# Kernel optimization log

Measured on AMD Instinct MI355X. Metric: run time of the kernel, lower is better.

Reference implementation:

```python
import jax, jax.numpy as jnp
import numpy as np

N = 8192
E = 262144
NEG = 0.2  # leaky_relu negative slope used throughout


def setup_inputs() -> dict:
    key = jax.random.key(0)
    def rn(i, shape, s=0.05):
        return jax.random.normal(jax.random.fold_in(key, i), shape, jnp.float32) * s
    d = {}
    d["x"] = jax.random.normal(jax.random.fold_in(key, 0), (N, 64), jnp.float32)
    d["edge_index"] = jax.random.randint(jax.random.fold_in(key, 1), (2, E), 0, N, dtype=jnp.int32)
    wshapes = {"w0": (64, 256), "as0": (4, 64), "ad0": (4, 64), "r0": (64, 256),
               "w1": (256, 256), "as1": (4, 64), "ad1": (4, 64), "r1": (256, 256),
               "w2": (256, 64), "as2": (1, 64), "ad2": (1, 64), "r2": (256, 64),
               "p0": (256, 64), "p1": (256, 64),
               "qw": (64, 64), "kw": (64, 64), "vw": (64, 64), "ow": (64, 64),
               "m1w": (64, 64), "m2w": (64, 32), "m3w": (32, 10)}
    for i, (nm, sh) in enumerate(wshapes.items()):
        d[nm] = rn(i + 2, sh)
    for nm, dim in [("g0", 256), ("g1", 256), ("g2", 64)]:
        d[nm] = jnp.ones((dim,), jnp.float32)
    for nm, dim in [("be0", 256), ("be1", 256), ("be2", 64), ("b0", 256), ("b1", 256), ("b2", 64),
                    ("qb", 64), ("kb", 64), ("vb", 64), ("ob", 64), ("m1b", 64), ("m2b", 32), ("m3b", 10)]:
        d[nm] = jnp.zeros((dim,), jnp.float32)
    return d


def _forward(edge_index, x, w0, as0, ad0, b0, g0, be0, r0,
             w1, as1, ad1, b1, g1, be1, r1,
             w2, as2, ad2, b2, g2, be2, r2,
             p0, p1, qw, qb, kw, kb, vw, vb, ow, ob,
             m1w, m1b, m2w, m2b, m3w, m3b):
    n = x.shape[0]
    loops = jnp.arange(n, dtype=edge_index.dtype)
    src = jnp.concatenate([edge_index[0], loops])  # add_self_loops=True
    dst = jnp.concatenate([edge_index[1], loops])

    def gat(h, w, a_s, a_d, b, heads):
        hw = (h @ w).reshape(n, heads, 64)  # [N, H, C]
        # PyG GATConv: e_ij = leaky_relu(att_src . h_j + att_dst . h_i), softmax over in-edges of i
        e = jax.nn.leaky_relu(jnp.sum(hw * a_s, -1)[src] + jnp.sum(hw * a_d, -1)[dst], NEG)  # [Etot, H]
        m = jax.ops.segment_max(e, dst, num_segments=n)
        ex = jnp.exp(e - m[dst])
        den = jax.ops.segment_sum(ex, dst, num_segments=n)
        alpha = ex / (den[dst] + 1e-16)
        out = jax.ops.segment_sum(hw[src] * alpha[:, :, None], dst, num_segments=n)
        return out.reshape(n, heads * 64) + b

    def bn(h, g, bta):  # BatchNorm1d, batch statistics (training-mode math)
        mu = jnp.mean(h, 0)
        var = jnp.var(h, 0)
        return (h - mu) * jax.lax.rsqrt(var + 1e-5) * g + bta

    outs = []
    h = x
    for (w, a_s, a_d, b, g, bt, r, heads) in [
            (w0, as0, ad0, b0, g0, be0, r0, 4),
            (w1, as1, ad1, b1, g1, be1, r1, 4),
            (w2, as2, ad2, b2, g2, be2, r2, 1)]:
        res = h @ r
        h = bn(gat(h, w, a_s, a_d, b, heads), g, bt) + res  # shapes always match here
        h = jax.nn.leaky_relu(h, NEG)
        outs.append(h)

    # JumpingKnowledge 'max' after projecting first two layers to hidden dim
    z = jnp.maximum(jnp.maximum(outs[0] @ p0, outs[1] @ p1), outs[2])  # [N, 64]

    # MultiHeadSelfAttention over all nodes (batch=1 implicit), 2 heads, head_dim=32
    q = (z @ qw + qb).reshape(n, 2, 32)
    k = (z @ kw + kb).reshape(n, 2, 32)
    v = (z @ vw + vb).reshape(n, 2, 32)
    attn = jax.nn.softmax(jnp.einsum('nhd,mhd->hnm', q, k) * (32 ** -0.5), axis=-1)
    z = jnp.einsum('hnm,mhd->nhd', attn, v).reshape(n, 64) @ ow + ob

    # MLP head (no data.batch -> GlobalAttention pool skipped)
    z = jax.nn.leaky_relu(z @ m1w + m1b, NEG)
    z = jax.nn.leaky_relu(z @ m2w + m2b, NEG)
    return z @ m3w + m3b


def reference(x, edge_index, w0, as0, ad0, b0, g0, be0, r0,
              w1, as1, ad1, b1, g1, be1, r1,
              w2, as2, ad2, b2, g2, be2, r2,
              p0, p1, qw, qb, kw, kb, vw, vb, ow, ob,
              m1w, m1b, m2w, m2b, m3w, m3b):
    return _forward(edge_index, x, w0, as0, ad0, b0, g0, be0, r0,
                    w1, as1, ad1, b1, g1, be1, r1,
                    w2, as2, ad2, b2, g2, be2, r2,
                    p0, p1, qw, qb, kw, kb, vw, vb, ow, ob,
                    m1w, m1b, m2w, m2b, m3w, m3b)
```

## Files before the change

kernel.cpp:

```cpp
#include <hip/hip_runtime.h>
#include <hip/hip_bf16.h>


#define NEG 0.2f
#define LOG2E 1.4426950408889634f

__device__ __forceinline__ float leaky(float v) { return v > 0.f ? v : NEG * v; }

__device__ __forceinline__ unsigned bf16u(float x) {
    unsigned u = __float_as_uint(x);
    u += 0x7FFFu + ((u >> 16) & 1u);
    return u >> 16;
}
__device__ __forceinline__ unsigned fmap(float f) {
    unsigned u = __float_as_uint(f);
    return (u & 0x80000000u) ? ~u : (u | 0x80000000u);
}
__device__ __forceinline__ float funmap(unsigned u) {
    unsigned b = (u & 0x80000000u) ? (u & 0x7FFFFFFFu) : ~u;
    return __uint_as_float(b);
}
__device__ __forceinline__ float fexp2(float x) {
#if __has_builtin(__builtin_amdgcn_exp2f)
    return __builtin_amdgcn_exp2f(x);
#else
    return exp2f(x);
#endif
}
__device__ __forceinline__ unsigned cvtpk(float lo, float hi) {
    unsigned r;
    asm("v_cvt_pk_bf16_f32 %0, %1, %2" : "=v"(r) : "v"(lo), "v"(hi));
    return r;
}

typedef __attribute__((ext_vector_type(8))) short bf16x8;
typedef __attribute__((ext_vector_type(16))) float f32x16;
typedef __attribute__((ext_vector_type(4))) unsigned uint4v;

__device__ __forceinline__ void split1(float v, unsigned& hb, unsigned& lb) {
    hb = bf16u(v);
    float hf = __uint_as_float(hb << 16);
    lb = bf16u(v - hf);
}

__global__ void split_rows(const float* __restrict__ in,
                           unsigned short* __restrict__ hi,
                           unsigned short* __restrict__ lo, int total4)
{
    int i = blockIdx.x * 256 + threadIdx.x;
    if (i >= total4) return;
    float4 v = ((const float4*)in)[i];
    float vv[4] = {v.x, v.y, v.z, v.w};
    ushort4 h, l;
#pragma unroll
    for (int j = 0; j < 4; ++j) {
        unsigned hb, lb;
        split1(vv[j], hb, lb);
        (&h.x)[j] = (unsigned short)hb;
        (&l.x)[j] = (unsigned short)lb;
    }
    ((ushort4*)hi)[i] = h;
    ((ushort4*)lo)[i] = l;
}

struct WEnt { const float* src; unsigned short* hi; unsigned short* lo; int K; int N; };
struct WArr { WEnt e[15]; };

__global__ void split_weights(WArr a)
{
    WEnt w = a.e[blockIdx.y];
    int id = blockIdx.x * 256 + threadIdx.x;
    if (id >= w.K * w.N) return;
    int k = id / w.N, n = id - k * w.N;
    unsigned hb, lb;
    split1(w.src[id], hb, lb);
    w.hi[(size_t)n * w.K + k] = (unsigned short)hb;
    w.lo[(size_t)n * w.K + k] = (unsigned short)lb;
}

__global__ __launch_bounds__(256) void gemm_mfma(
    const unsigned short* __restrict__ Ahi, const unsigned short* __restrict__ Alo,
    const unsigned short* __restrict__ Bhi, const unsigned short* __restrict__ Blo,
    const float* __restrict__ bias, float* __restrict__ C,
    unsigned short* __restrict__ Chi, unsigned short* __restrict__ Clo,
    const float* __restrict__ jkB, const float* __restrict__ jkC,
    unsigned* __restrict__ kmaxDst, const float* __restrict__ kbias,
    int M, int N, int K, int act)
{
    const int lane = threadIdx.x & 63, wid = threadIdx.x >> 6;
    const int hb4 = lane >> 5, lq = lane & 31;
    const int row0 = blockIdx.y * 64 + (wid >> 1) * 32;
    const int col0 = blockIdx.x * 64 + (wid & 1) * 32;
    const size_t abase = (size_t)(row0 + lq) * K + hb4 * 8;
    const size_t bbase = (size_t)(col0 + lq) * K + hb4 * 8;
    f32x16 acc0, acc1;
#pragma unroll
    for (int r = 0; r < 16; ++r) { acc0[r] = 0.f; acc1[r] = 0.f; }
    for (int k0 = 0; k0 < K; k0 += 16) {
        bf16x8 a_h = *(const bf16x8*)(Ahi + abase + k0);
        bf16x8 a_l = *(const bf16x8*)(Alo + abase + k0);
        bf16x8 b_h = *(const bf16x8*)(Bhi + bbase + k0);
        bf16x8 b_l = *(const bf16x8*)(Blo + bbase + k0);
        acc0 = __builtin_amdgcn_mfma_f32_32x32x16_bf16(a_h, b_h, acc0, 0, 0, 0);
        acc1 = __builtin_amdgcn_mfma_f32_32x32x16_bf16(a_l, b_h, acc1, 0, 0, 0);
        acc1 = __builtin_amdgcn_mfma_f32_32x32x16_bf16(a_h, b_l, acc1, 0, 0, 0);
    }
    int col = col0 + lq;
    if (col >= N) return;
    float bs = bias ? bias[col] : 0.f;
    float kmx = 0.f;
#pragma unroll
    for (int r = 0; r < 16; ++r) {
        int row = row0 + (r & 3) + 8 * (r >> 2) + 4 * hb4;
        float v = acc0[r] + acc1[r] + bs;
        if (act) v = leaky(v);
        if (jkB) v = fmaxf(fmaxf(v, jkB[(size_t)row * N + col]),
                           jkC[(size_t)row * N + col]);
        if (kmaxDst) kmx = fmaxf(kmx, fabsf(v + kbias[col & 63]));
        if (C) C[(size_t)row * N + col] = v;
        if (Chi) {
            unsigned hh, ll;
            split1(v, hh, ll);
            Chi[(size_t)row * N + col] = (unsigned short)hh;
            Clo[(size_t)row * N + col] = (unsigned short)ll;
        }
    }
    if (kmaxDst && col >= 64 && col < 128)
        atomicMax(&kmaxDst[col - 64], __float_as_uint(kmx));
}

template <int H>
__global__ __launch_bounds__(256) void sd_kernel(
    const float* __restrict__ hwres, int S,
    const float* __restrict__ a_s, const float* __restrict__ a_d,
    float* __restrict__ sval, float* __restrict__ dval,
    unsigned* __restrict__ svmax, int Nn)
{
    int i = blockIdx.x * 256 + threadIdx.x;
    int n = i / H, h = i & (H - 1);
    const float4* row = (const float4*)(hwres + (size_t)n * S + h * 64);
    const float4* as4 = (const float4*)(a_s + h * 64);
    const float4* ad4 = (const float4*)(a_d + h * 64);
    float s = 0.f, d = 0.f;
#pragma unroll
    for (int c = 0; c < 16; ++c) {
        float4 x = row[c], a = as4[c], b = ad4[c];
        s += x.x * a.x + x.y * a.y + x.z * a.z + x.w * a.w;
        d += x.x * b.x + x.y * b.y + x.z * b.z + x.w * b.w;
    }
    s *= LOG2E;
    d *= LOG2E;
    sval[i] = s;
    dval[i] = d;
    float m = s;
#pragma unroll
    for (int off = H; off < 64; off <<= 1) m = fmaxf(m, __shfl_xor(m, off));
    if ((threadIdx.x & 63) < H) atomicMax(&svmax[h], fmap(m));
}

__global__ void csr_count(const int* __restrict__ ei, int* __restrict__ cnt, int E) {
    int i = blockIdx.x * 256 + threadIdx.x;
    if (i < E) atomicAdd(&cnt[ei[E + i]], 1);
}

__global__ __launch_bounds__(256) void csr_scan(const int* __restrict__ cnt,
                                                int* __restrict__ rowptr,
                                                int* __restrict__ fill, int Nn)
{
    __shared__ int part[256];
    int t = threadIdx.x;
    int loc[32];
    int s = 0;
#pragma unroll
    for (int j = 0; j < 32; ++j) { loc[j] = s; s += cnt[t * 32 + j]; }
    part[t] = s;
    __syncthreads();
    for (int d = 1; d < 256; d <<= 1) {
        int v = (t >= d) ? part[t - d] : 0;
        __syncthreads();
        part[t] += v;
        __syncthreads();
    }
    int off = (t > 0) ? part[t - 1] : 0;
#pragma unroll
    for (int j = 0; j < 32; ++j) {
        int v = off + loc[j];
        rowptr[t * 32 + j] = v;
        fill[t * 32 + j] = v;
    }
    if (t == 255) rowptr[Nn] = part[255];
}

__global__ void csr_scatter(const int* __restrict__ ei, int* __restrict__ fill,
                            int* __restrict__ srcidx, int E) {
    int i = blockIdx.x * 256 + threadIdx.x;
    if (i < E) {
        int d = ei[E + i];
        int p = atomicAdd(&fill[d], 1);
        srcidx[p] = ei[i];
    }
}

__global__ __launch_bounds__(256) void gat_gather4(
    const int* __restrict__ rowptr, const int* __restrict__ srcidx,
    const float* __restrict__ hwres, int S,
    const float* __restrict__ sval, const float* __restrict__ dval,
    const unsigned* __restrict__ svmax, float* __restrict__ gout, int Nn)
{
    const int node = blockIdx.x * 4 + (threadIdx.x >> 6);
    const int lane = threadIdx.x & 63;
    const int hd = lane >> 4;
    const int cb = lane * 4;
    const int beg = rowptr[node], end = rowptr[node + 1];
    const float dv = dval[node * 4 + hd];
    const float B = leaky(funmap(svmax[hd]) + dv);
    float p = fexp2(leaky(sval[node * 4 + hd] + dv) - B);
    float l = p;
    float4 hv = *(const float4*)(hwres + (size_t)node * S + cb);
    float a0 = p * hv.x, a1 = p * hv.y, a2 = p * hv.z, a3 = p * hv.w;
    int i = beg;
    for (; i + 4 <= end; i += 4) {
        int s0 = srcidx[i], s1 = srcidx[i + 1];
        int s2 = srcidx[i + 2], s3 = srcidx[i + 3];
        float p0 = fexp2(leaky(sval[s0 * 4 + hd] + dv) - B);
        float p1 = fexp2(leaky(sval[s1 * 4 + hd] + dv) - B);
        float p2 = fexp2(leaky(sval[s2 * 4 + hd] + dv) - B);
        float p3 = fexp2(leaky(sval[s3 * 4 + hd] + dv) - B);
        float4 r0 = *(const float4*)(hwres + (size_t)s0 * S + cb);
        float4 r1 = *(const float4*)(hwres + (size_t)s1 * S + cb);
        float4 r2 = *(const float4*)(hwres + (size_t)s2 * S + cb);
        float4 r3 = *(const float4*)(hwres + (size_t)s3 * S + cb);
        l += (p0 + p1) + (p2 + p3);
        a0 += p0 * r0.x + p1 * r1.x + p2 * r2.x + p3 * r3.x;
        a1 += p0 * r0.y + p1 * r1.y + p2 * r2.y + p3 * r3.y;
        a2 += p0 * r0.z + p1 * r1.z + p2 * r2.z + p3 * r3.z;
        a3 += p0 * r0.w + p1 * r1.w + p2 * r2.w + p3 * r3.w;
    }
    for (; i < end; ++i) {
        int s0 = srcidx[i];
        float p0 = fexp2(leaky(sval[s0 * 4 + hd] + dv) - B);
        float4 r0 = *(const float4*)(hwres + (size_t)s0 * S + cb);
        l += p0;
        a0 += p0 * r0.x; a1 += p0 * r0.y; a2 += p0 * r0.z; a3 += p0 * r0.w;
    }
    float inv = 1.f / l;
    *(float4*)(gout + (size_t)node * 256 + cb) =
        make_float4(a0 * inv, a1 * inv, a2 * inv, a3 * inv);
}

__global__ __launch_bounds__(256) void gat_gather1(
    const int* __restrict__ rowptr, const int* __restrict__ srcidx,
    const float* __restrict__ hwres, int S,
    const float* __restrict__ sval, const float* __restrict__ dval,
    const unsigned* __restrict__ svmax, float* __restrict__ gout, int Nn)
{
    const int node = blockIdx.x * 4 + (threadIdx.x >> 6);
    const int lane = threadIdx.x & 63;
    const int beg = rowptr[node], end = rowptr[node + 1];
    const float dv = dval[node];
    const float B = leaky(funmap(svmax[0]) + dv);
    float p = fexp2(leaky(sval[node] + dv) - B);
    float l = p;
    float acc = p * hwres[(size_t)node * S + lane];
    int i = beg;
    for (; i + 4 <= end; i += 4) {
        int s0 = srcidx[i], s1 = srcidx[i + 1];
        int s2 = srcidx[i + 2], s3 = srcidx[i + 3];
        float p0 = fexp2(leaky(sval[s0] + dv) - B);
        float p1 = fexp2(leaky(sval[s1] + dv) - B);
        float p2 = fexp2(leaky(sval[s2] + dv) - B);
        float p3 = fexp2(leaky(sval[s3] + dv) - B);
        l += (p0 + p1) + (p2 + p3);
        acc += p0 * hwres[(size_t)s0 * S + lane] + p1 * hwres[(size_t)s1 * S + lane]
             + p2 * hwres[(size_t)s2 * S + lane] + p3 * hwres[(size_t)s3 * S + lane];
    }
    for (; i < end; ++i) {
        int s0 = srcidx[i];
        float p0 = fexp2(leaky(sval[s0] + dv) - B);
        l += p0;
        acc += p0 * hwres[(size_t)s0 * S + lane];
    }
    gout[(size_t)node * 64 + lane] = acc / l;
}

__global__ void bn_partial(const float* __restrict__ gout, double* __restrict__ sums,
                           int Nn, int C)
{
    int t = threadIdx.x;
    int c = t % C, sub = t / C, nsub = blockDim.x / C;
    int rbase = blockIdx.x * 32;
    double s = 0.0, sq = 0.0;
    for (int r = rbase + sub; r < rbase + 32; r += nsub) {
        float x = gout[(size_t)r * C + c];
        s += x;
        sq += (double)x * x;
    }
    atomicAdd(&sums[c], s);
    atomicAdd(&sums[C + c], sq);
}

__global__ void bn_res_act(const float* __restrict__ gout,
                           const float* __restrict__ hwres, int S, int logC,
                           const double* __restrict__ bnsum, double invN,
                           const float* __restrict__ g, const float* __restrict__ be,
                           float* __restrict__ outp,
                           unsigned short* __restrict__ shi,
                           unsigned short* __restrict__ slo, int total)
{
    int i = blockIdx.x * blockDim.x + threadIdx.x;
    if (i >= total) return;
    int C = 1 << logC;
    int c = i & (C - 1), row = i >> logC;
    double m = bnsum[c] * invN;
    double var = bnsum[C + c] * invN - m * m;
    float mu = (float)m;
    float rstd = (float)(1.0 / sqrt(var + 1e-5));
    float v = (gout[i] - mu) * rstd * g[c] + be[c]
              + hwres[(size_t)row * S + C + c];
    v = leaky(v);
    if (outp) outp[i] = v;
    if (shi) {
        unsigned hb, lb;
        split1(v, hb, lb);
        shi[i] = (unsigned short)hb;
        slo[i] = (unsigned short)lb;
    }
}

__global__ void qkv_prep(const float* __restrict__ zqkv,
                         const float* __restrict__ qb, const float* __restrict__ kb,
                         const float* __restrict__ vb,
                         const unsigned* __restrict__ kmaxu,
                         __hip_bfloat16* __restrict__ Qb, __hip_bfloat16* __restrict__ Kb,
                         __hip_bfloat16* __restrict__ Vf, float* __restrict__ bound,
                         int N)
{
    int idx = blockIdx.x * 256 + threadIdx.x;
    if (idx < 2 * N) {
        int h = idx / N, row = idx - h * N;
        const float scale = 0.17677669529663687f * LOG2E;
        const float* qp = zqkv + (size_t)row * 192 + h * 32;
        const float* kp = zqkv + (size_t)row * 192 + 64 + h * 32;
        float b = 0.f;
        unsigned qo[16], ko[16];
#pragma unroll
        for (int i = 0; i < 16; ++i) {
            float q0 = (qp[2 * i] + qb[h * 32 + 2 * i]) * scale;
            float q1 = (qp[2 * i + 1] + qb[h * 32 + 2 * i + 1]) * scale;
            float k0 = kp[2 * i] + kb[h * 32 + 2 * i];
            float k1 = kp[2 * i + 1] + kb[h * 32 + 2 * i + 1];
            b += fabsf(q0) * __uint_as_float(kmaxu[h * 32 + 2 * i]);
            b += fabsf(q1) * __uint_as_float(kmaxu[h * 32 + 2 * i + 1]);
            qo[i] = bf16u(q0) | (bf16u(q1) << 16);
            ko[i] = bf16u(k0) | (bf16u(k1) << 16);
        }
        uint4* qd = (uint4*)(Qb + (size_t)idx * 32);
        uint4* kd = (uint4*)(Kb + (size_t)idx * 32);
#pragma unroll
        for (int i = 0; i < 4; ++i) {
            qd[i] = make_uint4(qo[4 * i], qo[4 * i + 1], qo[4 * i + 2], qo[4 * i + 3]);
            kd[i] = make_uint4(ko[4 * i], ko[4 * i + 1], ko[4 * i + 2], ko[4 * i + 3]);
        }
        bound[idx] = b;
    } else {
        int j = idx - 2 * N;
        if (j >= 2 * (N >> 4) * 64) return;
        int lane = j & 63;
        int g = (j >> 6) % (N >> 4);
        int h = (j >> 6) / (N >> 4);
        int hi = lane >> 5;
        int kbase = g * 16 + 4 * hi;
        int d = (lane & 31) + h * 32;
        float bd = vb[d];
        unsigned o[4];
#pragma unroll
        for (int i = 0; i < 4; ++i) {
            int r0 = kbase + ((2 * i) & 3) + 8 * (i >> 1);
            unsigned u0 = bf16u(zqkv[(size_t)r0 * 192 + 128 + d] + bd);
            unsigned u1 = bf16u(zqkv[(size_t)(r0 + 1) * 192 + 128 + d] + bd);
            o[i] = u0 | (u1 << 16);
        }
        *(uint4*)(Vf + (size_t)j * 8) = make_uint4(o[0], o[1], o[2], o[3]);
    }
}

__global__ __launch_bounds__(256) void attn_mfma(
    const __hip_bfloat16* __restrict__ Qb, const __hip_bfloat16* __restrict__ Kb,
    const __hip_bfloat16* __restrict__ Vf, const float* __restrict__ bound,
    float* __restrict__ pl, __hip_bfloat16* __restrict__ pacc,
    int N, int nchunk, int chunksz)
{
    const int lane = threadIdx.x & 63;
    const int wid = threadIdx.x >> 6;
    const int hi = lane >> 5, lq = lane & 31;
    const int chunk = blockIdx.x;
    const int qtile = blockIdx.y * 4 + wid;
    const int head = qtile / (N >> 5);
    const int q0 = (qtile % (N >> 5)) * 32;
    const int kbase = chunk * chunksz;

    const size_t qrow = (size_t)head * N + q0 + lq;
    const bf16x8 qf0 = *(const bf16x8*)(Qb + qrow * 32 + hi * 8);
    const bf16x8 qf1 = *(const bf16x8*)(Qb + qrow * 32 + hi * 8 + 16);
    const float bnd = bound[qrow];

    f32x16 oacc;
#pragma unroll
    for (int r = 0; r < 16; ++r) oacc[r] = 0.f;
    float lsum = 0.f;

    for (int kt = kbase; kt < kbase + chunksz; kt += 32) {
        const size_t krow = (size_t)head * N + kt + lq;
        const bf16x8 kf0 = *(const bf16x8*)(Kb + krow * 32 + hi * 8);
        const bf16x8 kf1 = *(const bf16x8*)(Kb + krow * 32 + hi * 8 + 16);
        f32x16 s;
#pragma unroll
        for (int r = 0; r < 16; ++r) s[r] = 0.f;
        s = __builtin_amdgcn_mfma_f32_32x32x16_bf16(kf0, qf0, s, 0, 0, 0);
        s = __builtin_amdgcn_mfma_f32_32x32x16_bf16(kf1, qf1, s, 0, 0, 0);
        const __hip_bfloat16* vfb =
            Vf + (((size_t)head * (N >> 4) + (kt >> 4)) * 64 + lane) * 8;
        const bf16x8 vf0 = *(const bf16x8*)vfb;
        const bf16x8 vf1 = *(const bf16x8*)(vfb + 64 * 8);

        float p[16];
#pragma unroll
        for (int r = 0; r < 16; ++r) p[r] = fexp2(s[r] - bnd);
        float ls = 0.f;
#pragma unroll
        for (int r = 0; r < 16; ++r) ls += p[r];
        lsum += ls;

        uint4v b1, b2;
        b1[0] = cvtpk(p[0], p[1]);
        b1[1] = cvtpk(p[2], p[3]);
        b1[2] = cvtpk(p[4], p[5]);
        b1[3] = cvtpk(p[6], p[7]);
        b2[0] = cvtpk(p[8], p[9]);
        b2[1] = cvtpk(p[10], p[11]);
        b2[2] = cvtpk(p[12], p[13]);
        b2[3] = cvtpk(p[14], p[15]);
        oacc = __builtin_amdgcn_mfma_f32_32x32x16_bf16(
            vf0, __builtin_bit_cast(bf16x8, b1), oacc, 0, 0, 0);
        oacc = __builtin_amdgcn_mfma_f32_32x32x16_bf16(
            vf1, __builtin_bit_cast(bf16x8, b2), oacc, 0, 0, 0);
    }
    lsum += __shfl_xor(lsum, 32);
    const size_t hr = (size_t)head * N + q0 + lq;
    if (hi == 0) pl[hr * nchunk + chunk] = lsum;
    __hip_bfloat16* pb = pacc + (hr * nchunk + chunk) * 32;
#pragma unroll
    for (int rg = 0; rg < 4; ++rg) {
        unsigned lo = cvtpk(oacc[rg * 4 + 0], oacc[rg * 4 + 1]);
        unsigned hw2 = cvtpk(oacc[rg * 4 + 2], oacc[rg * 4 + 3]);
        *(uint2*)(pb + rg * 8 + hi * 4) = make_uint2(lo, hw2);
    }
}

__global__ void attn_combine(const float* __restrict__ pl,
                             const __hip_bfloat16* __restrict__ pacc,
                             unsigned short* __restrict__ shi,
                             unsigned short* __restrict__ slo, int N, int nchunk)
{
    int i = blockIdx.x * blockDim.x + threadIdx.x;
    if (i >= 2 * N * 32) return;
    int hr = i >> 5, cc = i & 31;
    float l = 0.f, a = 0.f;
    for (int c = 0; c < nchunk; ++c) {
        l += pl[(size_t)hr * nchunk + c];
        a += __bfloat162float(pacc[((size_t)hr * nchunk + c) * 32 + cc]);
    }
    int head = hr / N, row = hr - head * N;
    float v = a / l;
    size_t oi = (size_t)row * 64 + head * 32 + cc;
    unsigned hb, lb;
    split1(v, hb, lb);
    shi[oi] = (unsigned short)hb;
    slo[oi] = (unsigned short)lb;
}

extern "C" void kernel_launch(void* const* d_in, const int* in_sizes, int n_in,
                              void* d_out, int out_size, void* d_ws, size_t ws_size,
                              hipStream_t stream)
{
    const float* x = (const float*)d_in[0];
    const int* ei = (const int*)d_in[1];
    const float* w[3]   = {(const float*)d_in[2], (const float*)d_in[6],  (const float*)d_in[10]};
    const float* as_[3] = {(const float*)d_in[3], (const float*)d_in[7],  (const float*)d_in[11]};
    const float* ad_[3] = {(const float*)d_in[4], (const float*)d_in[8],  (const float*)d_in[12]};
    const float* rw[3]  = {(const float*)d_in[5], (const float*)d_in[9],  (const float*)d_in[13]};
    const float* p0 = (const float*)d_in[14];
    const float* p1 = (const float*)d_in[15];
    const float* qw = (const float*)d_in[16];
    const float* kw = (const float*)d_in[17];
    const float* vw = (const float*)d_in[18];
    const float* ow = (const float*)d_in[19];
    const float* m1w = (const float*)d_in[20];
    const float* m2w = (const float*)d_in[21];
    const float* m3w = (const float*)d_in[22];
    const float* g_[3]  = {(const float*)d_in[23], (const float*)d_in[24], (const float*)d_in[25]};
    const float* be_[3] = {(const float*)d_in[26], (const float*)d_in[27], (const float*)d_in[28]};
    const float* qb  = (const float*)d_in[32];
    const float* kb  = (const float*)d_in[33];
    const float* vb  = (const float*)d_in[34];
    const float* ob  = (const float*)d_in[35];
    const float* m1b = (const float*)d_in[36];
    const float* m2b = (const float*)d_in[37];
    const float* m3b = (const float*)d_in[38];

    const int N = in_sizes[0] / 64;
    const int E = in_sizes[1] / 2;

    float* ws = (float*)d_ws;
    size_t off = 0;
    auto alloc = [&](size_t n) {
        float* p = ws + off;
        off += (n + 255) & ~(size_t)255;
        return p;
    };
    float* hwres = alloc((size_t)N * 512);
    float* gout  = alloc((size_t)N * 256);
    unsigned short* sChi = (unsigned short*)alloc((size_t)N * 128);
    unsigned short* sClo = (unsigned short*)alloc((size_t)N * 128);
    float* h2   = alloc((size_t)N * 64);
    float* sval = alloc((size_t)N * 4);
    float* dval = alloc((size_t)N * 4);
    size_t ms_begin = off;
    int* cnt = (int*)alloc(N);
    double* bnsum = (double*)alloc(3 * 1024);
    unsigned* kmaxu = (unsigned*)alloc(64);
    unsigned* svmax = (unsigned*)alloc(16);
    size_t ms_end = off;
    int* rowptr = (int*)alloc(N + 256);
    int* fill   = (int*)alloc(N);
    int* srcidx = (int*)alloc(E);
    unsigned short* sAhi = (unsigned short*)alloc((size_t)N * 128);
    unsigned short* sAlo = (unsigned short*)alloc((size_t)N * 128);
    unsigned short* sBhi = (unsigned short*)alloc((size_t)N * 32);
    unsigned short* sBlo = (unsigned short*)alloc((size_t)N * 32);
    unsigned short* G0h = (unsigned short*)alloc(512 * 64 / 2);
    unsigned short* G0l = (unsigned short*)alloc(512 * 64 / 2);
    unsigned short* G1h = (unsigned short*)alloc(512 * 256 / 2);
    unsigned short* G1l = (unsigned short*)alloc(512 * 256 / 2);
    unsigned short* G2h = (unsigned short*)alloc(128 * 256 / 2);
    unsigned short* G2l = (unsigned short*)alloc(128 * 256 / 2);
    unsigned short* P0h = (unsigned short*)alloc(64 * 256 / 2);
    unsigned short* P0l = (unsigned short*)alloc(64 * 256 / 2);
    unsigned short* P1h = (unsigned short*)alloc(64 * 256 / 2);
    unsigned short* P1l = (unsigned short*)alloc(64 * 256 / 2);
    unsigned short* Gqh = (unsigned short*)alloc(192 * 64 / 2);
    unsigned short* Gql = (unsigned short*)alloc(192 * 64 / 2);
    unsigned short* Owh = (unsigned short*)alloc(64 * 64 / 2);
    unsigned short* Owl = (unsigned short*)alloc(64 * 64 / 2);
    unsigned short* M1h = (unsigned short*)alloc(64 * 64 / 2);
    unsigned short* M1l = (unsigned short*)alloc(64 * 64 / 2);
    unsigned short* M2h = (unsigned short*)alloc(64 * 64 / 2);
    unsigned short* M2l = (unsigned short*)alloc(64 * 64 / 2);
    unsigned short* M3h = (unsigned short*)alloc(64 * 32 / 2);
    unsigned short* M3l = (unsigned short*)alloc(64 * 32 / 2);
    float* zqkv = hwres;
    __hip_bfloat16* pacc = (__hip_bfloat16*)(hwres + (size_t)N * 192);
    float* tA = gout;
    float* tB = gout + (size_t)N * 64;
    const int NCHUNK = 8;
    __hip_bfloat16* Qb = (__hip_bfloat16*)sChi;
    __hip_bfloat16* Kb = Qb + (size_t)2 * N * 32;
    __hip_bfloat16* Vf = Kb + (size_t)2 * N * 32;
    float* boundArr = (float*)(Vf + (size_t)2 * N * 32);
    float* pl = h2;

    {
        WArr wa;
        wa.e[0]  = WEnt{w[0],  G0h,              G0l,              64, 256};
        wa.e[1]  = WEnt{rw[0], G0h + 256 * 64,   G0l + 256 * 64,   64, 256};
        wa.e[2]  = WEnt{w[1],  G1h,              G1l,              256, 256};
        wa.e[3]  = WEnt{rw[1], G1h + 256 * 256,  G1l + 256 * 256,  256, 256};
        wa.e[4]  = WEnt{w[2],  G2h,              G2l,              256, 64};
        wa.e[5]  = WEnt{rw[2], G2h + 64 * 256,   G2l + 64 * 256,   256, 64};
        wa.e[6]  = WEnt{p0,    P0h,              P0l,              256, 64};
        wa.e[7]  = WEnt{p1,    P1h,              P1l,              256, 64};
        wa.e[8]  = WEnt{qw,    Gqh,              Gql,              64, 64};
        wa.e[9]  = WEnt{kw,    Gqh + 64 * 64,    Gql + 64 * 64,    64, 64};
        wa.e[10] = WEnt{vw,    Gqh + 128 * 64,   Gql + 128 * 64,   64, 64};
        wa.e[11] = WEnt{ow,    Owh,              Owl,              64, 64};
        wa.e[12] = WEnt{m1w,   M1h,              M1l,              64, 64};
        wa.e[13] = WEnt{m2w,   M2h,              M2l,              64, 32};
        wa.e[14] = WEnt{m3w,   M3h,              M3l,              32, 10};
        split_weights<<<dim3(256, 15), 256, 0, stream>>>(wa);
    }
    hipMemsetAsync(ws + ms_begin, 0, (ms_end - ms_begin) * 4, stream);
    csr_count<<<(E + 255) / 256, 256, 0, stream>>>(ei, cnt, E);
    csr_scan<<<1, 256, 0, stream>>>(cnt, rowptr, fill, N);
    csr_scatter<<<(E + 255) / 256, 256, 0, stream>>>(ei, fill, srcidx, E);
    split_rows<<<(N * 64 / 4 + 255) / 256, 256, 0, stream>>>(x, sAhi, sAlo, N * 64 / 4);

    auto gemmM = [&](const unsigned short* Ah, const unsigned short* Al,
                     const unsigned short* Bh, const unsigned short* Bl,
                     const float* bias, float* C, unsigned short* Chi,
                     unsigned short* Clo, const float* jkB, const float* jkC,
                     unsigned* kmx, const float* kbias,
                     int M, int Nc, int K, int act) {
        dim3 grid((Nc + 63) / 64, M / 64);
        gemm_mfma<<<grid, 256, 0, stream>>>(Ah, Al, Bh, Bl, bias, C, Chi, Clo,
                                            jkB, jkC, kmx, kbias, M, Nc, K, act);
    };

    const unsigned short* inh[3] = {sAhi, sChi, sAhi};
    const unsigned short* inl[3] = {sAlo, sClo, sAlo};
    unsigned short* outh[3] = {sChi, sAhi, nullptr};
    unsigned short* outl[3] = {sClo, sAlo, nullptr};
    const unsigned short* Gh[3] = {G0h, G1h, G2h};
    const unsigned short* Gl[3] = {G0l, G1l, G2l};
    int Ksz[3] = {64, 256, 256}, Csz[3] = {256, 256, 64}, logC[3] = {8, 8, 6};
    int Hh[3] = {4, 4, 1};

    for (int l = 0; l < 3; ++l) {
        int C = Csz[l], S = 2 * C;
        gemmM(inh[l], inl[l], Gh[l], Gl[l], nullptr, hwres, nullptr, nullptr,
              nullptr, nullptr, nullptr, nullptr, N, S, Ksz[l], 0);
        if (Hh[l] == 4) {
            sd_kernel<4><<<N * 4 / 256, 256, 0, stream>>>(
                hwres, S, as_[l], ad_[l], sval, dval, svmax + l * 4, N);
            gat_gather4<<<N / 4, 256, 0, stream>>>(
                rowptr, srcidx, hwres, S, sval, dval, svmax + l * 4, gout, N);
        } else {
            sd_kernel<1><<<N / 256, 256, 0, stream>>>(
                hwres, S, as_[l], ad_[l], sval, dval, svmax + l * 4, N);
            gat_gather1<<<N / 4, 256, 0, stream>>>(
                rowptr, srcidx, hwres, S, sval, dval, svmax + l * 4, gout, N);
        }
        double* bns = bnsum + l * 512;
        bn_partial<<<N / 32, 256, 0, stream>>>(gout, bns, N, C);
        bn_res_act<<<((size_t)N * C) / 256, 256, 0, stream>>>(
            gout, hwres, S, logC[l], bns, 1.0 / (double)N, g_[l], be_[l],
            l == 2 ? h2 : nullptr, outh[l], outl[l], N * C);
    }

    gemmM(sAhi, sAlo, P1h, P1l, nullptr, tB, nullptr, nullptr,
          nullptr, nullptr, nullptr, nullptr, N, 64, 256, 0);
    gemmM(sChi, sClo, P0h, P0l, nullptr, nullptr, sBhi, sBlo,
          tB, h2, nullptr, nullptr, N, 64, 256, 0);

    gemmM(sBhi, sBlo, Gqh, Gql, nullptr, zqkv, nullptr, nullptr,
          nullptr, nullptr, kmaxu, kb, N, 192, 64, 0);

    int ptot = 2 * N + 2 * (N >> 4) * 64;
    qkv_prep<<<(ptot + 255) / 256, 256, 0, stream>>>(
        zqkv, qb, kb, vb, kmaxu, Qb, Kb, Vf, boundArr, N);
    attn_mfma<<<dim3(NCHUNK, (2 * N / 32) / 4), 256, 0, stream>>>(
        Qb, Kb, Vf, boundArr, pl, pacc, N, NCHUNK, N / NCHUNK);
    attn_combine<<<(2 * N * 32 + 255) / 256, 256, 0, stream>>>(
        pl, pacc, sAhi, sAlo, N, NCHUNK);

    gemmM(sAhi, sAlo, Owh, Owl, ob, tA, sBhi, sBlo,
          nullptr, nullptr, nullptr, nullptr, N, 64, 64, 0);
    gemmM(sBhi, sBlo, M1h, M1l, m1b, nullptr, sAhi, sAlo,
          nullptr, nullptr, nullptr, nullptr, N, 64, 64, 1);
    gemmM(sAhi, sAlo, M2h, M2l, m2b, nullptr, sBhi, sBlo,
          nullptr, nullptr, nullptr, nullptr, N, 32, 64, 1);
    gemmM(sBhi, sBlo, M3h, M3l, m3b, (float*)d_out, nullptr, nullptr,
          nullptr, nullptr, nullptr, nullptr, N, 10, 32, 0);
}
```

Measured before the change: 397.7 us.

## Prefetch next K/V tiles in attention loop and double key-chunk split

The attention MFMA loop now loads the next iteration's K and V fragments into registers before computing on the current ones, so global-load latency can overlap the MFMA and exp work. The key dimension is also split into 16 chunks instead of 8, giving twice as many blocks for better GPU occupancy. In exchange, the combine step has more partials to merge and the kernel uses more registers. The partial-accumulator buffer is moved to the start of the reused workspace to fit the larger size.

Measured after the change: 408.6 us. +2.7%, slower.

```diff
diff --git a/kernel.cpp b/kernel.cpp
--- a/kernel.cpp
+++ b/kernel.cpp
@@ -398,6 +398,7 @@
     const int head = qtile / (N >> 5);
     const int q0 = (qtile % (N >> 5)) * 32;
     const int kbase = chunk * chunksz;
+    const int kend = kbase + chunksz;
 
     const size_t qrow = (size_t)head * N + q0 + lq;
     const bf16x8 qf0 = *(const bf16x8*)(Qb + qrow * 32 + hi * 8);
@@ -409,19 +410,32 @@
     for (int r = 0; r < 16; ++r) oacc[r] = 0.f;
     float lsum = 0.f;
 
-    for (int kt = kbase; kt < kbase + chunksz; kt += 32) {
-        const size_t krow = (size_t)head * N + kt + lq;
-        const bf16x8 kf0 = *(const bf16x8*)(Kb + krow * 32 + hi * 8);
-        const bf16x8 kf1 = *(const bf16x8*)(Kb + krow * 32 + hi * 8 + 16);
+    size_t krow = (size_t)head * N + kbase + lq;
+    bf16x8 kf0 = *(const bf16x8*)(Kb + krow * 32 + hi * 8);
+    bf16x8 kf1 = *(const bf16x8*)(Kb + krow * 32 + hi * 8 + 16);
+    const __hip_bfloat16* vfb0 =
+        Vf + (((size_t)head * (N >> 4) + (kbase >> 4)) * 64 + lane) * 8;
+    bf16x8 vf0 = *(const bf16x8*)vfb0;
+    bf16x8 vf1 = *(const bf16x8*)(vfb0 + 512);
+
+    for (int kt = kbase; kt < kend; kt += 32) {
+        bf16x8 kf0n = kf0, kf1n = kf1, vf0n = vf0, vf1n = vf1;
+        int ktn = kt + 32;
+        if (ktn < kend) {
+            size_t krn = (size_t)head * N + ktn + lq;
+            kf0n = *(const bf16x8*)(Kb + krn * 32 + hi * 8);
+            kf1n = *(const bf16x8*)(Kb + krn * 32 + hi * 8 + 16);
+            const __hip_bfloat16* vfn =
+                Vf + (((size_t)head * (N >> 4) + (ktn >> 4)) * 64 + lane) * 8;
+            vf0n = *(const bf16x8*)vfn;
+            vf1n = *(const bf16x8*)(vfn + 512);
+        }
+
         f32x16 s;
 #pragma unroll
         for (int r = 0; r < 16; ++r) s[r] = 0.f;
         s = __builtin_amdgcn_mfma_f32_32x32x16_bf16(kf0, qf0, s, 0, 0, 0);
         s = __builtin_amdgcn_mfma_f32_32x32x16_bf16(kf1, qf1, s, 0, 0, 0);
-        const __hip_bfloat16* vfb =
-            Vf + (((size_t)head * (N >> 4) + (kt >> 4)) * 64 + lane) * 8;
-        const bf16x8 vf0 = *(const bf16x8*)vfb;
-        const bf16x8 vf1 = *(const bf16x8*)(vfb + 64 * 8);
 
         float p[16];
 #pragma unroll
@@ -444,6 +458,8 @@
             vf0, __builtin_bit_cast(bf16x8, b1), oacc, 0, 0, 0);
         oacc = __builtin_amdgcn_mfma_f32_32x32x16_bf16(
             vf1, __builtin_bit_cast(bf16x8, b2), oacc, 0, 0, 0);
+
+        kf0 = kf0n; kf1 = kf1n; vf0 = vf0n; vf1 = vf1n;
     }
     lsum += __shfl_xor(lsum, 32);
     const size_t hr = (size_t)head * N + q0 + lq;
@@ -559,10 +575,10 @@
     unsigned short* M3h = (unsigned short*)alloc(64 * 32 / 2);
     unsigned short* M3l = (unsigned short*)alloc(64 * 32 / 2);
     float* zqkv = hwres;
-    __hip_bfloat16* pacc = (__hip_bfloat16*)(hwres + (size_t)N * 192);
+    const int NCHUNK = 16;
+    __hip_bfloat16* pacc = (__hip_bfloat16*)hwres;
     float* tA = gout;
     float* tB = gout + (size_t)N * 64;
-    const int NCHUNK = 8;
     __hip_bfloat16* Qb = (__hip_bfloat16*)sChi;
     __hip_bfloat16* Kb = Qb + (size_t)2 * N * 32;
     __hip_bfloat16* Vf = Kb + (size_t)2 * N * 32;
```
